# Performance work log

Measured on AMD Instinct MI355X. Metric: run time of the kernel, lower is better.

Reference implementation:

```python
import jax, jax.numpy as jnp
import numpy as np

N_E = 8192
E_DIM = 256
N_TOK = 32768
MU = 0.25  # commitment weight; beta=0 so diversity loss is skipped


def setup_inputs() -> dict:
    key = jax.random.key(0)
    k1, k2, k3 = jax.random.split(key, 3)
    x = jax.random.normal(k1, (N_TOK, E_DIM), dtype=jnp.float32)
    # codebook init: uniform(-1/n_e, 1/n_e) as in the torch module
    emb = jax.random.uniform(k2, (N_E, E_DIM), dtype=jnp.float32,
                             minval=-1.0 / N_E, maxval=1.0 / N_E)
    label = jax.random.randint(k3, (N_TOK,), 0, 10, dtype=jnp.int32)
    return {"x": x, "emb": emb, "label": label, "idx": 0}


def reference(x, emb, label, idx):
    # latent: [N, e_dim]
    latent = x.reshape(-1, emb.shape[1])
    # pairwise squared distances via norm + matmul: [N, n_e]
    d = (jnp.sum(latent * latent, axis=1, keepdims=True)
         + jnp.sum(emb * emb, axis=1)[None, :]
         - 2.0 * (latent @ emb.T))
    indices = jnp.argmin(d, axis=-1)                 # [N]
    x_q = emb[indices].reshape(x.shape)              # gather
    commitment_loss = jnp.mean(jnp.square(jax.lax.stop_gradient(x_q) - x))
    codebook_loss = jnp.mean(jnp.square(x_q - jax.lax.stop_gradient(x)))
    loss = codebook_loss + MU * commitment_loss      # beta=0 -> no diversity term
    x_q_out = x + jax.lax.stop_gradient(x_q - x)     # straight-through estimator
    return x_q_out, loss, indices.reshape(x.shape[:-1])
```

## Files before the change

### kernel.cpp

```cpp
#include <hip/hip_runtime.h>
#include <float.h>
#include <stdint.h>

#define N_TOK 32768
#define N_E   8192
#define EDIM  256
#define MU_W  0.25f
#define NSPLIT 4
#define NRANGE 2048
#define BM 128
#define NTILES 16
#define MARGIN_F 2048.0f
#define XSCALE 512.0f
#define ESCALE -131072.0f

typedef _Float16 f16;
typedef _Float16 f16x8 __attribute__((ext_vector_type(8)));
typedef _Float16 f16x4 __attribute__((ext_vector_type(4)));
typedef float f32x4 __attribute__((ext_vector_type(4)));
typedef unsigned int u32;

#define WS_EMB16   0
#define WS_SX      4194304
#define WS_SE      4325376
#define WS_SE25    4358144
#define WS_CAND    4390912
#define WS_PART    6488064
#define WS_RCNT    6619136
#define WS_RLIST   6619392
#define WS_X16     6750464
#define WS_NEED_FULL 23527680ull

__device__ inline void gload_lds16(const void* g, void* l) {
  __builtin_amdgcn_global_load_lds(
      (const __attribute__((address_space(1))) unsigned int*)g,
      (__attribute__((address_space(3))) unsigned int*)l, 16, 0, 0);
}

__device__ inline u32 umin_(u32 a, u32 b) { return a < b ? a : b; }
__device__ inline u32 umax_(u32 a, u32 b) { return a > b ? a : b; }

__device__ inline void ins4(u32 v, u32& a, u32& b, u32& c, u32& d) {
  u32 mn = umin_(v, a), mx = umax_(v, a);  a = mn;
  u32 mn2 = umin_(mx, b), mx2 = umax_(mx, b); b = mn2;
  u32 mn3 = umin_(mx2, c), mx3 = umax_(mx2, c); c = mn3;
  d = umin_(mx3, d);
}

__device__ inline u32 fmap(float f) {
  u32 b = __float_as_uint(f);
  u32 m = (u32)((int)b >> 31) | 0x80000000u;
  return b ^ m;
}
__device__ inline float funmap(u32 u) {
  u32 b = (u & 0x80000000u) ? (u ^ 0x80000000u) : ~u;
  return __uint_as_float(b);
}

__global__ void zero_kernel(u32* p) { p[0] = 0u; }

__global__ __launch_bounds__(256) void conv_kernel(const float* __restrict__ src,
                                                   char* __restrict__ dst16,
                                                   float* __restrict__ norms,
                                                   float* __restrict__ norms25,
                                                   float scale, int write16, int nrows) {
  int wave = threadIdx.x >> 6;
  int lane = threadIdx.x & 63;
  int row = blockIdx.x * 4 + wave;
  if (row >= nrows) return;
  const float4 v = *(const float4*)(src + (size_t)row * EDIM + lane * 4);
  float s = (v.x * v.x + v.y * v.y) + (v.z * v.z + v.w * v.w);
#pragma unroll
  for (int off = 32; off >= 1; off >>= 1) s += __shfl_xor(s, off);
  if (lane == 0) {
    norms[row] = s;
    if (norms25) norms25[row] = s * 0x1p25f;
  }
  if (write16) {
    f16x4 h;
    h[0] = (f16)(v.x * scale); h[1] = (f16)(v.y * scale);
    h[2] = (f16)(v.z * scale); h[3] = (f16)(v.w * scale);
    int sw = (row & 7) << 4;
    *(f16x4*)(dst16 + (size_t)row * 512 + ((lane * 8) ^ sw)) = h;
  }
}

template<bool XF16>
__global__ __launch_bounds__(256, 2) void vq_main(const float* __restrict__ xf,
                                                  const char* __restrict__ x16,
                                                  const char* __restrict__ e16,
                                                  const float* __restrict__ se25,
                                                  u32* __restrict__ cand) {
  __shared__ f16 Abuf[128 * 128];
  __shared__ f16 Bbuf[128 * 128];
  __shared__ u32 scratch[4][4][16][4];

  const int tid = threadIdx.x;
  const int lane = tid & 63;
  const int wid = tid >> 6;
  const int wm = wid >> 1, wn = wid & 1;
  const int l15 = lane & 15;
  const int lg = lane >> 4;
  const int split = blockIdx.x & 3;
  const int bm = (blockIdx.x >> 2) * BM;
  const int nbase = split * NRANGE;

  u32 d1[16], d2[16], d3[16], d4[16];
#pragma unroll
  for (int s = 0; s < 16; ++s) { d1[s] = 0xFFFFFFFFu; d2[s] = 0xFFFFFFFFu; d3[s] = 0xFFFFFFFFu; d4[s] = 0xFFFFFFFFu; }

  for (int t = 0; t < NTILES; ++t) {
    const int n0 = nbase + t * 128;

    float sev[4];
#pragma unroll
    for (int ni = 0; ni < 4; ++ni) sev[ni] = se25[n0 + wn * 64 + ni * 16 + l15];

    f32x4 acc[4][4];
#pragma unroll
    for (int mi = 0; mi < 4; ++mi)
#pragma unroll
      for (int ni = 0; ni < 4; ++ni)
        acc[mi][ni] = (f32x4){sev[ni], sev[ni], sev[ni], sev[ni]};

#pragma unroll
    for (int h = 0; h < 2; ++h) {
      __syncthreads();
      {
        const char* bbase = e16 + (size_t)(nbase + t * 128) * 512 + h * 256;
#pragma unroll
        for (int it = 0; it < 8; ++it) {
          int c = wid * 8 + it;
          int Lrel = c * 1024 + lane * 16;
          int col = Lrel >> 8, p = Lrel & 255;
          gload_lds16(bbase + col * 512 + p, (char*)Bbuf + c * 1024);
        }
      }
      if (XF16) {
        const char* abase = x16 + (size_t)bm * 512 + h * 256;
#pragma unroll
        for (int it = 0; it < 8; ++it) {
          int c = wid * 8 + it;
          int Lrel = c * 1024 + lane * 16;
          int col = Lrel >> 8, p = Lrel & 255;
          gload_lds16(abase + col * 512 + p, (char*)Abuf + c * 1024);
        }
      } else {
        int row = tid >> 1, sub = tid & 1;
        const float4* xs = (const float4*)xf + (size_t)(bm + row) * 64 + h * 32 + sub * 16;
        char* ab = (char*)Abuf + row * 256;
        int sw = (row & 7) << 4;
#pragma unroll
        for (int q = 0; q < 8; ++q) {
          float4 a0 = xs[q * 2], a1 = xs[q * 2 + 1];
          f16x8 hv;
          hv[0] = (f16)(a0.x * XSCALE); hv[1] = (f16)(a0.y * XSCALE);
          hv[2] = (f16)(a0.z * XSCALE); hv[3] = (f16)(a0.w * XSCALE);
          hv[4] = (f16)(a1.x * XSCALE); hv[5] = (f16)(a1.y * XSCALE);
          hv[6] = (f16)(a1.z * XSCALE); hv[7] = (f16)(a1.w * XSCALE);
          *(f16x8*)(ab + ((sub * 128 + q * 16) ^ sw)) = hv;
        }
      }
      __syncthreads();

#pragma unroll
      for (int kk = 0; kk < 4; ++kk) {
        f16x8 av[4], bv[4];
#pragma unroll
        for (int mi = 0; mi < 4; ++mi) {
          int ar = wm * 64 + mi * 16 + l15;
          av[mi] = *(const f16x8*)((const char*)Abuf + ar * 256 +
                                   ((kk * 64 + lg * 16) ^ ((ar & 7) << 4)));
        }
#pragma unroll
        for (int ni = 0; ni < 4; ++ni) {
          int br = wn * 64 + ni * 16 + l15;
          bv[ni] = *(const f16x8*)((const char*)Bbuf + br * 256 +
                                   ((kk * 64 + lg * 16) ^ ((br & 7) << 4)));
        }
#pragma unroll
        for (int mi = 0; mi < 4; ++mi)
#pragma unroll
          for (int ni = 0; ni < 4; ++ni)
            acc[mi][ni] = __builtin_amdgcn_mfma_f32_16x16x32_f16(av[mi], bv[ni], acc[mi][ni], 0, 0, 0);
      }
    }

#pragma unroll
    for (int ni = 0; ni < 4; ++ni) {
      u32 id = (u32)((t << 7) | (wn << 6) | (ni << 4) | l15);
#pragma unroll
      for (int mi = 0; mi < 4; ++mi)
#pragma unroll
        for (int r = 0; r < 4; ++r) {
          u32 up = (fmap(acc[mi][ni][r]) & 0xFFFFF800u) | id;
          int s = mi * 4 + r;
          ins4(up, d1[s], d2[s], d3[s], d4[s]);
        }
    }
  }

#pragma unroll
  for (int off = 8; off >= 1; off >>= 1) {
#pragma unroll
    for (int s = 0; s < 16; ++s) {
      u32 e1 = (u32)__shfl_xor((int)d1[s], off);
      u32 e2 = (u32)__shfl_xor((int)d2[s], off);
      u32 e3 = (u32)__shfl_xor((int)d3[s], off);
      u32 e4 = (u32)__shfl_xor((int)d4[s], off);
      ins4(e1, d1[s], d2[s], d3[s], d4[s]);
      ins4(e2, d1[s], d2[s], d3[s], d4[s]);
      ins4(e3, d1[s], d2[s], d3[s], d4[s]);
      ins4(e4, d1[s], d2[s], d3[s], d4[s]);
    }
  }
  if (l15 == 0) {
#pragma unroll
    for (int s = 0; s < 16; ++s) {
      scratch[wid][lg][s][0] = d1[s];
      scratch[wid][lg][s][1] = d2[s];
      scratch[wid][lg][s][2] = d3[s];
      scratch[wid][lg][s][3] = d4[s];
    }
  }
  __syncthreads();
  if (tid < 128) {
    int row = tid;
    int wmr = row >> 6, mi = (row >> 4) & 3, lgr = (row >> 2) & 3, rr = row & 3;
    int s = mi * 4 + rr;
    u32 a1 = scratch[wmr * 2 + 0][lgr][s][0];
    u32 a2 = scratch[wmr * 2 + 0][lgr][s][1];
    u32 a3 = scratch[wmr * 2 + 0][lgr][s][2];
    u32 a4 = scratch[wmr * 2 + 0][lgr][s][3];
    ins4(scratch[wmr * 2 + 1][lgr][s][0], a1, a2, a3, a4);
    ins4(scratch[wmr * 2 + 1][lgr][s][1], a1, a2, a3, a4);
    ins4(scratch[wmr * 2 + 1][lgr][s][2], a1, a2, a3, a4);
    ins4(scratch[wmr * 2 + 1][lgr][s][3], a1, a2, a3, a4);
    size_t base = (size_t)split * (N_TOK * 4) + (size_t)(bm + row) * 4;
    cand[base + 0] = a1; cand[base + 1] = a2; cand[base + 2] = a3; cand[base + 3] = a4;
  }
}

__global__ __launch_bounds__(256) void vq_gather_kernel(
    const float* __restrict__ x, const float* __restrict__ emb,
    const float* __restrict__ sx, const float* __restrict__ se,
    const u32* __restrict__ cand,
    float* __restrict__ out_q, float* __restrict__ out_idx,
    float* __restrict__ partials,
    u32* __restrict__ rcnt, u32* __restrict__ rlist) {
  const int token = blockIdx.x;
  const int tid = threadIdx.x;
  __shared__ int s_j;
  __shared__ int s_cnt;
  __shared__ int s_cj[16];
  __shared__ float s_dv[16];
  __shared__ float red[4];

  if (tid == 0) {
    u32 u[16];
    float uf[16];
    float gmin = FLT_MAX;
#pragma unroll
    for (int sp = 0; sp < 4; ++sp)
#pragma unroll
      for (int c = 0; c < 4; ++c) {
        u32 v = cand[(size_t)sp * (N_TOK * 4) + (size_t)token * 4 + c];
        u[sp * 4 + c] = v;
        float f = funmap(v);
        uf[sp * 4 + c] = f;
        gmin = fminf(gmin, f);
      }
    bool guard = false;
#pragma unroll
    for (int sp = 0; sp < 4; ++sp) guard = guard || (uf[sp * 4 + 3] <= gmin + MARGIN_F);
    int cnt;
    if (guard) {
      u32 slot = atomicAdd(rcnt, 1u);
      rlist[slot] = (u32)token;
      cnt = -1;
    } else {
      cnt = 0;
#pragma unroll
      for (int sp = 0; sp < 4; ++sp)
#pragma unroll
        for (int c = 0; c < 4; ++c) {
          int k = sp * 4 + c;
          if (uf[k] <= gmin + MARGIN_F) {
            u32 idx = u[k] & 0x7FFu;
            int col = (int)((idx >> 7) & 15) * 128 + (int)((idx >> 6) & 1) * 64 +
                      (int)((idx >> 4) & 3) * 16 + (int)(idx & 15);
            s_cj[cnt++] = sp * NRANGE + col;
          }
        }
      if (cnt == 1) s_j = s_cj[0];
    }
    s_cnt = cnt;
  }
  __syncthreads();
  int cnt = s_cnt;
  if (cnt < 0) return;
  if (cnt > 1 && tid < cnt) {
    int j = s_cj[tid];
    const float* xr = x + (size_t)token * EDIM;
    const float* er = emb + (size_t)j * EDIM;
    float a = 0.f;
    for (int k = 0; k < EDIM; ++k) a = fmaf(xr[k], er[k], a);
    s_dv[tid] = (sx[token] + se[j]) - 2.0f * a;
  }
  __syncthreads();
  if (cnt > 1 && tid == 0) {
    float bd = s_dv[0]; int bj = s_cj[0];
    for (int c = 1; c < cnt; ++c) {
      float d = s_dv[c]; int j = s_cj[c];
      if (d < bd || (d == bd && j < bj)) { bd = d; bj = j; }
    }
    s_j = bj;
  }
  __syncthreads();
  const int j = s_j;
  if (tid == 0) out_idx[token] = (float)j;
  float xv = x[(size_t)token * EDIM + tid];
  float q  = emb[(size_t)j * EDIM + tid];
  float diff = q - xv;
  out_q[(size_t)token * EDIM + tid] = xv + diff;
  float sq = diff * diff;
#pragma unroll
  for (int off = 32; off >= 1; off >>= 1) sq += __shfl_xor(sq, off);
  const int wave = tid >> 6, lane = tid & 63;
  if (lane == 0) red[wave] = sq;
  __syncthreads();
  if (tid == 0) partials[token] = (red[0] + red[1]) + (red[2] + red[3]);
}

__global__ __launch_bounds__(256) void vq_rescan_kernel(
    const float* __restrict__ x, const float* __restrict__ emb,
    const float* __restrict__ sx, const float* __restrict__ se,
    const u32* __restrict__ rcnt, const u32* __restrict__ rlist,
    float* __restrict__ out_q, float* __restrict__ out_idx,
    float* __restrict__ partials) {
  const int tid = threadIdx.x;
  const int n = (int)rcnt[0];
  __shared__ float xs[EDIM];
  __shared__ float rd[4];
  __shared__ int   rj[4];
  __shared__ int   s_bj;

  for (int it = blockIdx.x; it < n; it += gridDim.x) {
    const int token = (int)rlist[it];
    xs[tid] = x[(size_t)token * EDIM + tid];
    __syncthreads();
    const float sxt = sx[token];
    float bd = FLT_MAX; int bj = 0;
    for (int c = 0; c < N_E / 256; ++c) {
      int j = tid * (N_E / 256) + c;
      const float* er = emb + (size_t)j * EDIM;
      float a = 0.f;
      for (int k = 0; k < EDIM; ++k) a = fmaf(xs[k], er[k], a);
      float d = (sxt + se[j]) - 2.0f * a;
      if (d < bd || (d == bd && j < bj)) { bd = d; bj = j; }
    }
    const int lane = tid & 63, wave = tid >> 6;
#pragma unroll
    for (int off = 32; off >= 1; off >>= 1) {
      float d2 = __shfl_xor(bd, off);
      int   j2 = __shfl_xor(bj, off);
      if (d2 < bd || (d2 == bd && j2 < bj)) { bd = d2; bj = j2; }
    }
    if (lane == 0) { rd[wave] = bd; rj[wave] = bj; }
    __syncthreads();
    if (tid == 0) {
      float bbd = rd[0]; int bbj = rj[0];
#pragma unroll
      for (int w = 1; w < 4; ++w) {
        if (rd[w] < bbd || (rd[w] == bbd && rj[w] < bbj)) { bbd = rd[w]; bbj = rj[w]; }
      }
      s_bj = bbj;
      out_idx[token] = (float)bbj;
    }
    __syncthreads();
    const int j = s_bj;
    float xv = xs[tid];
    float q  = emb[(size_t)j * EDIM + tid];
    float diff = q - xv;
    out_q[(size_t)token * EDIM + tid] = xv + diff;
    float sq = diff * diff;
#pragma unroll
    for (int off = 32; off >= 1; off >>= 1) sq += __shfl_xor(sq, off);
    if (lane == 0) rd[wave] = sq;
    __syncthreads();
    if (tid == 0) partials[token] = (rd[0] + rd[1]) + (rd[2] + rd[3]);
    __syncthreads();
  }
}

__global__ __launch_bounds__(256) void vq_loss_kernel(const float* __restrict__ partials,
                                                      float* __restrict__ loss_out) {
  const int tid = threadIdx.x;
  float s = 0.f;
  for (int i = tid; i < N_TOK; i += 256) s += partials[i];
  __shared__ float red[4];
#pragma unroll
  for (int off = 32; off >= 1; off >>= 1) s += __shfl_xor(s, off);
  const int wave = tid >> 6, lane = tid & 63;
  if (lane == 0) red[wave] = s;
  __syncthreads();
  if (tid == 0) {
    float tot = (red[0] + red[1]) + (red[2] + red[3]);
    float mean = tot / (float)(N_TOK * EDIM);
    loss_out[0] = mean + MU_W * mean;
  }
}

extern "C" void kernel_launch(void* const* d_in, const int* in_sizes, int n_in,
                              void* d_out, int out_size, void* d_ws, size_t ws_size,
                              hipStream_t stream) {
  const float* x   = (const float*)d_in[0];
  const float* emb = (const float*)d_in[1];

  float* out      = (float*)d_out;
  float* out_q    = out;
  float* out_loss = out + (size_t)N_TOK * EDIM;
  float* out_idx  = out_loss + 1;

  char* w = (char*)d_ws;
  char*  emb16    = w + WS_EMB16;
  float* sx       = (float*)(w + WS_SX);
  float* se       = (float*)(w + WS_SE);
  float* se25     = (float*)(w + WS_SE25);
  u32*   cand     = (u32*)(w + WS_CAND);
  float* partials = (float*)(w + WS_PART);
  u32*   rcnt     = (u32*)(w + WS_RCNT);
  u32*   rlist    = (u32*)(w + WS_RLIST);
  char*  x16      = w + WS_X16;

  const bool xf16 = (ws_size >= WS_NEED_FULL);

  zero_kernel<<<1, 1, 0, stream>>>(rcnt);
  conv_kernel<<<N_E / 4, 256, 0, stream>>>(emb, emb16, se, se25, ESCALE, 1, N_E);
  conv_kernel<<<N_TOK / 4, 256, 0, stream>>>(x, x16, sx, nullptr, XSCALE, xf16 ? 1 : 0, N_TOK);

  if (xf16)
    vq_main<true><<<NSPLIT * (N_TOK / BM), 256, 0, stream>>>(x, x16, emb16, se25, cand);
  else
    vq_main<false><<<NSPLIT * (N_TOK / BM), 256, 0, stream>>>(x, x16, emb16, se25, cand);

  vq_gather_kernel<<<N_TOK, 256, 0, stream>>>(x, emb, sx, se, cand, out_q, out_idx, partials,
                                              rcnt, rlist);
  vq_rescan_kernel<<<256, 256, 0, stream>>>(x, emb, sx, se, rcnt, rlist, out_q, out_idx, partials);
  vq_loss_kernel<<<1, 256, 0, stream>>>(partials, out_loss);
}
```

Measured before the change: 330.8 us.

## Restructure VQ distance kernel with resident A tile, double-buffered B, med3 top-4

The main distance kernel now uses 512 threads with a 128x256 output tile. The whole 128x256 fp16 x-tile is converted once into LDS and stays there, while codebook K-chunks are double-buffered through global_load_lds so the next chunk is prefetched during compute. The top-4 selection switches to max-based insertion using v_med3_u32 on positive-offset float bits, which removes the fmap/funmap conversion and the column remapping in the gather step. The separate x fp16 conversion pass is dropped. In exchange LDS use grows and occupancy per CU may fall, and a wider margin lets more tokens fall into the rescan path.

```diff
diff --git a/kernel.cpp b/kernel.cpp
--- a/kernel.cpp
+++ b/kernel.cpp
@@ -8,9 +8,12 @@
 #define MU_W  0.25f
 #define NSPLIT 4
 #define NRANGE 2048
-#define BM 128
-#define NTILES 16
-#define MARGIN_F 2048.0f
+#define BMr 128
+#define BNr 256
+#define NT8 8
+#define TQ  4
+#define MARGIN_F 4096.0f
+#define OFFSETF (-0x1p21f)
 #define XSCALE 512.0f
 #define ESCALE -131072.0f
 
@@ -28,8 +31,6 @@
 #define WS_PART    6488064
 #define WS_RCNT    6619136
 #define WS_RLIST   6619392
-#define WS_X16     6750464
-#define WS_NEED_FULL 23527680ull
 
 __device__ inline void gload_lds16(const void* g, void* l) {
   __builtin_amdgcn_global_load_lds(
@@ -37,24 +38,21 @@
       (__attribute__((address_space(3))) unsigned int*)l, 16, 0, 0);
 }
 
+__device__ inline u32 umax_(u32 a, u32 b) { return a > b ? a : b; }
 __device__ inline u32 umin_(u32 a, u32 b) { return a < b ? a : b; }
-__device__ inline u32 umax_(u32 a, u32 b) { return a > b ? a : b; }
-
-__device__ inline void ins4(u32 v, u32& a, u32& b, u32& c, u32& d) {
-  u32 mn = umin_(v, a), mx = umax_(v, a);  a = mn;
-  u32 mn2 = umin_(mx, b), mx2 = umax_(mx, b); b = mn2;
-  u32 mn3 = umin_(mx2, c), mx3 = umax_(mx2, c); c = mn3;
-  d = umin_(mx3, d);
-}
-
-__device__ inline u32 fmap(float f) {
-  u32 b = __float_as_uint(f);
-  u32 m = (u32)((int)b >> 31) | 0x80000000u;
-  return b ^ m;
-}
-__device__ inline float funmap(u32 u) {
-  u32 b = (u & 0x80000000u) ? (u ^ 0x80000000u) : ~u;
-  return __uint_as_float(b);
+
+__device__ inline u32 med3u(u32 a, u32 b, u32 c) {
+  u32 r;
+  asm("v_med3_u32 %0, %1, %2, %3" : "=v"(r) : "v"(a), "v"(b), "v"(c));
+  return r;
+}
+
+__device__ inline void ins4max(u32 v, u32& a, u32& b, u32& c, u32& d) {
+  u32 na = umax_(a, v);
+  u32 nb = med3u(a, b, v);
+  u32 nc = med3u(b, c, v);
+  u32 nd = med3u(c, d, v);
+  a = na; b = nb; c = nc; d = nd;
 }
 
 __global__ void zero_kernel(u32* p) { p[0] = 0u; }
@@ -85,36 +83,61 @@
   }
 }
 
-template<bool XF16>
-__global__ __launch_bounds__(256, 2) void vq_main(const float* __restrict__ xf,
-                                                  const char* __restrict__ x16,
+__global__ __launch_bounds__(512, 2) void vq_main(const float* __restrict__ x,
                                                   const char* __restrict__ e16,
                                                   const float* __restrict__ se25,
                                                   u32* __restrict__ cand) {
-  __shared__ f16 Abuf[128 * 128];
-  __shared__ f16 Bbuf[128 * 128];
-  __shared__ u32 scratch[4][4][16][4];
+  __shared__ __align__(16) char Abuf[128 * 512];
+  __shared__ __align__(16) char Bbuf[2][256 * 128];
+  __shared__ u32 scratch[8][4][16][4];
 
   const int tid = threadIdx.x;
   const int lane = tid & 63;
   const int wid = tid >> 6;
-  const int wm = wid >> 1, wn = wid & 1;
+  const int wm = wid >> 2;
+  const int wn = wid & 3;
   const int l15 = lane & 15;
-  const int lg = lane >> 4;
+  const int lg  = lane >> 4;
   const int split = blockIdx.x & 3;
-  const int bm = (blockIdx.x >> 2) * BM;
+  const int bm = (blockIdx.x >> 2) * BMr;
   const int nbase = split * NRANGE;
 
+  {
+    const int row = tid >> 2, seg = tid & 3;
+    const float4* xs = (const float4*)(x + (size_t)(bm + row) * EDIM + seg * 64);
+    const int sw = (row & 7) << 4;
+    char* ab = Abuf + row * 512;
+#pragma unroll
+    for (int u = 0; u < 8; ++u) {
+      float4 a0 = xs[2 * u], a1 = xs[2 * u + 1];
+      f16x8 hv;
+      hv[0] = (f16)(a0.x * XSCALE); hv[1] = (f16)(a0.y * XSCALE);
+      hv[2] = (f16)(a0.z * XSCALE); hv[3] = (f16)(a0.w * XSCALE);
+      hv[4] = (f16)(a1.x * XSCALE); hv[5] = (f16)(a1.y * XSCALE);
+      hv[6] = (f16)(a1.z * XSCALE); hv[7] = (f16)(a1.w * XSCALE);
+      *(f16x8*)(ab + ((seg * 128 + u * 16) ^ sw)) = hv;
+    }
+  }
+  {
+    const char* src = e16 + (size_t)nbase * 512;
+#pragma unroll
+    for (int j = 0; j < 4; ++j) {
+      int tt = j * 512 + tid;
+      gload_lds16(src + (size_t)(tt >> 3) * 512 + (tt & 7) * 16, Bbuf[0] + tt * 16);
+    }
+  }
+  __syncthreads();
+
   u32 d1[16], d2[16], d3[16], d4[16];
 #pragma unroll
-  for (int s = 0; s < 16; ++s) { d1[s] = 0xFFFFFFFFu; d2[s] = 0xFFFFFFFFu; d3[s] = 0xFFFFFFFFu; d4[s] = 0xFFFFFFFFu; }
-
-  for (int t = 0; t < NTILES; ++t) {
-    const int n0 = nbase + t * 128;
-
+  for (int s = 0; s < 16; ++s) { d1[s] = 0u; d2[s] = 0u; d3[s] = 0u; d4[s] = 0u; }
+
+  int cur = 0;
+  for (int t = 0; t < NT8; ++t) {
     float sev[4];
 #pragma unroll
-    for (int ni = 0; ni < 4; ++ni) sev[ni] = se25[n0 + wn * 64 + ni * 16 + l15];
+    for (int ni = 0; ni < 4; ++ni)
+      sev[ni] = se25[nbase + t * 256 + wn * 64 + ni * 16 + l15] + OFFSETF;
 
     f32x4 acc[4][4];
 #pragma unroll
@@ -123,80 +146,55 @@
       for (int ni = 0; ni < 4; ++ni)
         acc[mi][ni] = (f32x4){sev[ni], sev[ni], sev[ni], sev[ni]};
 
-#pragma unroll
-    for (int h = 0; h < 2; ++h) {
-      __syncthreads();
-      {
-        const char* bbase = e16 + (size_t)(nbase + t * 128) * 512 + h * 256;
-#pragma unroll
-        for (int it = 0; it < 8; ++it) {
-          int c = wid * 8 + it;
-          int Lrel = c * 1024 + lane * 16;
-          int col = Lrel >> 8, p = Lrel & 255;
-          gload_lds16(bbase + col * 512 + p, (char*)Bbuf + c * 1024);
+    for (int q = 0; q < TQ; ++q) {
+      const int step = t * TQ + q;
+      if (step + 1 < NT8 * TQ) {
+        const int t2 = (step + 1) >> 2, q2 = (step + 1) & 3;
+        const char* src = e16 + (size_t)(nbase + t2 * 256) * 512 + q2 * 128;
+        char* dst = Bbuf[cur ^ 1];
+#pragma unroll
+        for (int j = 0; j < 4; ++j) {
+          int tt = j * 512 + tid;
+          gload_lds16(src + (size_t)(tt >> 3) * 512 + (tt & 7) * 16, dst + tt * 16);
         }
       }
-      if (XF16) {
-        const char* abase = x16 + (size_t)bm * 512 + h * 256;
-#pragma unroll
-        for (int it = 0; it < 8; ++it) {
-          int c = wid * 8 + it;
-          int Lrel = c * 1024 + lane * 16;
-          int col = Lrel >> 8, p = Lrel & 255;
-          gload_lds16(abase + col * 512 + p, (char*)Abuf + c * 1024);
+#pragma unroll
+      for (int kk = 0; kk < 2; ++kk) {
+        f16x8 av[4], bv[4];
+#pragma unroll
+        for (int mi = 0; mi < 4; ++mi) {
+          const int ar = wm * 64 + mi * 16 + l15;
+          av[mi] = *(const f16x8*)(Abuf + ar * 512 +
+                                   ((q * 128 + kk * 64 + lg * 16) ^ ((ar & 7) << 4)));
         }
-      } else {
-        int row = tid >> 1, sub = tid & 1;
-        const float4* xs = (const float4*)xf + (size_t)(bm + row) * 64 + h * 32 + sub * 16;
-        char* ab = (char*)Abuf + row * 256;
-        int sw = (row & 7) << 4;
-#pragma unroll
-        for (int q = 0; q < 8; ++q) {
-          float4 a0 = xs[q * 2], a1 = xs[q * 2 + 1];
-          f16x8 hv;
-          hv[0] = (f16)(a0.x * XSCALE); hv[1] = (f16)(a0.y * XSCALE);
-          hv[2] = (f16)(a0.z * XSCALE); hv[3] = (f16)(a0.w * XSCALE);
-          hv[4] = (f16)(a1.x * XSCALE); hv[5] = (f16)(a1.y * XSCALE);
-          hv[6] = (f16)(a1.z * XSCALE); hv[7] = (f16)(a1.w * XSCALE);
-          *(f16x8*)(ab + ((sub * 128 + q * 16) ^ sw)) = hv;
+#pragma unroll
+        for (int ni = 0; ni < 4; ++ni) {
+          const int br = wn * 64 + ni * 16 + l15;
+          bv[ni] = *(const f16x8*)(Bbuf[cur] + br * 128 +
+                                   ((kk * 64 + lg * 16) ^ ((br & 7) << 4)));
+        }
+#pragma unroll
+        for (int mi = 0; mi < 4; ++mi)
+#pragma unroll
+          for (int ni = 0; ni < 4; ++ni)
+            acc[mi][ni] = __builtin_amdgcn_mfma_f32_16x16x32_f16(av[mi], bv[ni], acc[mi][ni], 0, 0, 0);
+      }
+      if (q == TQ - 1) {
+#pragma unroll
+        for (int ni = 0; ni < 4; ++ni) {
+          const u32 id = (u32)((t << 8) | (wn << 6) | (ni << 4) | l15);
+#pragma unroll
+          for (int mi = 0; mi < 4; ++mi)
+#pragma unroll
+            for (int r = 0; r < 4; ++r) {
+              u32 up = (__float_as_uint(acc[mi][ni][r]) & 0xFFFFF800u) | id;
+              int s = mi * 4 + r;
+              ins4max(up, d1[s], d2[s], d3[s], d4[s]);
+            }
         }
       }
       __syncthreads();
-
-#pragma unroll
-      for (int kk = 0; kk < 4; ++kk) {
-        f16x8 av[4], bv[4];
-#pragma unroll
-        for (int mi = 0; mi < 4; ++mi) {
-          int ar = wm * 64 + mi * 16 + l15;
-          av[mi] = *(const f16x8*)((const char*)Abuf + ar * 256 +
-                                   ((kk * 64 + lg * 16) ^ ((ar & 7) << 4)));
-        }
-#pragma unroll
-        for (int ni = 0; ni < 4; ++ni) {
-          int br = wn * 64 + ni * 16 + l15;
-          bv[ni] = *(const f16x8*)((const char*)Bbuf + br * 256 +
-                                   ((kk * 64 + lg * 16) ^ ((br & 7) << 4)));
-        }
-#pragma unroll
-        for (int mi = 0; mi < 4; ++mi)
-#pragma unroll
-          for (int ni = 0; ni < 4; ++ni)
-            acc[mi][ni] = __builtin_amdgcn_mfma_f32_16x16x32_f16(av[mi], bv[ni], acc[mi][ni], 0, 0, 0);
-      }
-    }
-
-#pragma unroll
-    for (int ni = 0; ni < 4; ++ni) {
-      u32 id = (u32)((t << 7) | (wn << 6) | (ni << 4) | l15);
-#pragma unroll
-      for (int mi = 0; mi < 4; ++mi)
-#pragma unroll
-        for (int r = 0; r < 4; ++r) {
-          u32 up = (fmap(acc[mi][ni][r]) & 0xFFFFF800u) | id;
-          int s = mi * 4 + r;
-          ins4(up, d1[s], d2[s], d3[s], d4[s]);
-        }
+      cur ^= 1;
     }
   }
 
@@ -208,10 +206,10 @@
       u32 e2 = (u32)__shfl_xor((int)d2[s], off);
       u32 e3 = (u32)__shfl_xor((int)d3[s], off);
       u32 e4 = (u32)__shfl_xor((int)d4[s], off);
-      ins4(e1, d1[s], d2[s], d3[s], d4[s]);
-      ins4(e2, d1[s], d2[s], d3[s], d4[s]);
-      ins4(e3, d1[s], d2[s], d3[s], d4[s]);
-      ins4(e4, d1[s], d2[s], d3[s], d4[s]);
+      ins4max(e1, d1[s], d2[s], d3[s], d4[s]);
+      ins4max(e2, d1[s], d2[s], d3[s], d4[s]);
+      ins4max(e3, d1[s], d2[s], d3[s], d4[s]);
+      ins4max(e4, d1[s], d2[s], d3[s], d4[s]);
     }
   }
   if (l15 == 0) {
@@ -225,17 +223,19 @@
   }
   __syncthreads();
   if (tid < 128) {
-    int row = tid;
-    int wmr = row >> 6, mi = (row >> 4) & 3, lgr = (row >> 2) & 3, rr = row & 3;
-    int s = mi * 4 + rr;
-    u32 a1 = scratch[wmr * 2 + 0][lgr][s][0];
-    u32 a2 = scratch[wmr * 2 + 0][lgr][s][1];
-    u32 a3 = scratch[wmr * 2 + 0][lgr][s][2];
-    u32 a4 = scratch[wmr * 2 + 0][lgr][s][3];
-    ins4(scratch[wmr * 2 + 1][lgr][s][0], a1, a2, a3, a4);
-    ins4(scratch[wmr * 2 + 1][lgr][s][1], a1, a2, a3, a4);
-    ins4(scratch[wmr * 2 + 1][lgr][s][2], a1, a2, a3, a4);
-    ins4(scratch[wmr * 2 + 1][lgr][s][3], a1, a2, a3, a4);
+    const int row = tid;
+    const int wmr = row >> 6, mi = (row >> 4) & 3, lgr = (row >> 2) & 3, rr = row & 3;
+    const int s = mi * 4 + rr;
+    u32 a1 = scratch[wmr * 4][lgr][s][0];
+    u32 a2 = scratch[wmr * 4][lgr][s][1];
+    u32 a3 = scratch[wmr * 4][lgr][s][2];
+    u32 a4 = scratch[wmr * 4][lgr][s][3];
+#pragma unroll
+    for (int w = 1; w < 4; ++w) {
+#pragma unroll
+      for (int c = 0; c < 4; ++c)
+        ins4max(scratch[wmr * 4 + w][lgr][s][c], a1, a2, a3, a4);
+    }
     size_t base = (size_t)split * (N_TOK * 4) + (size_t)(bm + row) * 4;
     cand[base + 0] = a1; cand[base + 1] = a2; cand[base + 2] = a3; cand[base + 3] = a4;
   }
@@ -266,7 +266,7 @@
       for (int c = 0; c < 4; ++c) {
         u32 v = cand[(size_t)sp * (N_TOK * 4) + (size_t)token * 4 + c];
         u[sp * 4 + c] = v;
-        float f = funmap(v);
+        float f = __uint_as_float(v);
         uf[sp * 4 + c] = f;
         gmin = fminf(gmin, f);
       }
@@ -285,12 +285,8 @@
 #pragma unroll
         for (int c = 0; c < 4; ++c) {
           int k = sp * 4 + c;
-          if (uf[k] <= gmin + MARGIN_F) {
-            u32 idx = u[k] & 0x7FFu;
-            int col = (int)((idx >> 7) & 15) * 128 + (int)((idx >> 6) & 1) * 64 +
-                      (int)((idx >> 4) & 3) * 16 + (int)(idx & 15);
-            s_cj[cnt++] = sp * NRANGE + col;
-          }
+          if (uf[k] <= gmin + MARGIN_F)
+            s_cj[cnt++] = sp * NRANGE + (int)(u[k] & 0x7FFu);
         }
       if (cnt == 1) s_j = s_cj[0];
     }
@@ -431,18 +427,12 @@
   float* partials = (float*)(w + WS_PART);
   u32*   rcnt     = (u32*)(w + WS_RCNT);
   u32*   rlist    = (u32*)(w + WS_RLIST);
-  char*  x16      = w + WS_X16;
-
-  const bool xf16 = (ws_size >= WS_NEED_FULL);
 
   zero_kernel<<<1, 1, 0, stream>>>(rcnt);
   conv_kernel<<<N_E / 4, 256, 0, stream>>>(emb, emb16, se, se25, ESCALE, 1, N_E);
-  conv_kernel<<<N_TOK / 4, 256, 0, stream>>>(x, x16, sx, nullptr, XSCALE, xf16 ? 1 : 0, N_TOK);
-
-  if (xf16)
-    vq_main<true><<<NSPLIT * (N_TOK / BM), 256, 0, stream>>>(x, x16, emb16, se25, cand);
-  else
-    vq_main<false><<<NSPLIT * (N_TOK / BM), 256, 0, stream>>>(x, x16, emb16, se25, cand);
+  conv_kernel<<<N_TOK / 4, 256, 0, stream>>>(x, nullptr, sx, nullptr, XSCALE, 0, N_TOK);
+
+  vq_main<<<NSPLIT * (N_TOK / BMr), 512, 0, stream>>>(x, emb16, se25, cand);
 
   vq_gather_kernel<<<N_TOK, 256, 0, stream>>>(x, emb, sx, se, cand, out_q, out_idx, partials,
                                               rcnt, rlist);
```

After: 555.8 us. +68.0%, slower.
